# Performance work log

Hardware: AMD Instinct MI355X
Metric: run time of the kernel (lower is better)

The kernel has to match this reference:

```python
import jax, jax.numpy as jnp
import numpy as np

W, H = 512, 512
SHIFT_NORM = 100.0
P = 1
WEIGHT = 10.0
EPS = 1e-16


def _cv_matrix(angle, scale, shift, cx, cy):
    # cv2.getRotationMatrix2D-style matrix (pixel coords) with extra x-shift.
    alpha = scale * jnp.cos(angle)
    beta = scale * jnp.sin(angle)
    row0 = jnp.stack([alpha, beta, (1.0 - alpha) * cx - beta * cy + shift], axis=-1)
    row1 = jnp.stack([-beta, alpha, beta * cx + (1.0 - alpha) * cy], axis=-1)
    return jnp.stack([row0, row1], axis=-2)  # [B,2,3]


def _normalize_transform(M, width, height):
    # Convert pixel-space affine to normalized [-1,1] coords (align_corners=True).
    a, b, tx = M[:, 0, 0], M[:, 0, 1], M[:, 0, 2]
    c, d, ty = M[:, 1, 0], M[:, 1, 1], M[:, 1, 2]
    sw = float(width - 1)
    sh = float(height - 1)
    A = a
    Bc = b * sh / sw
    Cc = a + b * sh / sw + 2.0 * tx / sw - 1.0
    D = c * sw / sh
    E = d
    Fc = c * sw / sh + d + 2.0 * ty / sh - 1.0
    row0 = jnp.stack([A, Bc, Cc], axis=-1)
    row1 = jnp.stack([D, E, Fc], axis=-1)
    return jnp.stack([row0, row1], axis=-2)  # [B,2,3]


def _affine_grid(T, height, width):
    # torch affine_grid, align_corners=True
    u = jnp.linspace(-1.0, 1.0, width, dtype=T.dtype)
    v = jnp.linspace(-1.0, 1.0, height, dtype=T.dtype)
    vv, uu = jnp.meshgrid(v, u, indexing='ij')
    base = jnp.stack([uu, vv, jnp.ones_like(uu)], axis=-1)  # [H,W,3]
    return jnp.einsum('bij,hwj->bhwi', T, base)  # [B,H,W,2] (x,y)


def _grid_sample(img, grid):
    # bilinear, zeros padding, align_corners=True. img [B,C,H,W], grid [B,Ho,Wo,2]
    B, C, Hi, Wi = img.shape
    x = (grid[..., 0] + 1.0) * (Wi - 1) / 2.0
    y = (grid[..., 1] + 1.0) * (Hi - 1) / 2.0
    x0 = jnp.floor(x)
    y0 = jnp.floor(y)
    wx1 = x - x0
    wy1 = y - y0
    wx0 = 1.0 - wx1
    wy0 = 1.0 - wy1

    def gather(xi, yi):
        valid = ((xi >= 0) & (xi < Wi) & (yi >= 0) & (yi < Hi)).astype(img.dtype)
        xc = jnp.clip(xi, 0, Wi - 1).astype(jnp.int32)
        yc = jnp.clip(yi, 0, Hi - 1).astype(jnp.int32)
        g = jax.vmap(lambda im, xb, yb, vb: im[:, yb, xb] * vb[None])
        return g(img, xc, yc, valid)  # [B,C,Ho,Wo]

    out = (gather(x0, y0) * (wx0 * wy0)[:, None]
           + gather(x0 + 1, y0) * (wx1 * wy0)[:, None]
           + gather(x0, y0 + 1) * (wx0 * wy1)[:, None]
           + gather(x0 + 1, y0 + 1) * (wx1 * wy1)[:, None])
    return out


def setup_inputs() -> dict:
    key = jax.random.key(0)
    k1, k2, k3 = jax.random.split(key, 3)
    theta = jax.random.normal(k1, (32, 3), dtype=jnp.float32)
    img_R = jax.random.normal(k2, (32, 3, H, W), dtype=jnp.float32)
    img_R_orig = jax.random.normal(k3, (32, 3, H, W), dtype=jnp.float32)
    return {"theta": theta, "img_R": img_R, "img_R_orig": img_R_orig}


def reference(theta, img_R, img_R_orig):
    cx, cy = W // 2, H // 2
    M = _cv_matrix(theta[:, 0], theta[:, 1], SHIFT_NORM * theta[:, 2], cx, cy)
    T = _normalize_transform(M, W, H)
    grid = _affine_grid(T, H, W)
    warped = _grid_sample(img_R_orig, grid)
    mask = jnp.ones((img_R.shape[0], 1, H, W), dtype=img_R.dtype)
    warped_mask = _grid_sample(mask, grid)[:, 0]  # [B,H,W]
    # p=1 norm over channel dim
    nrm = jnp.sum(jnp.abs(img_R - warped), axis=1)  # [B,H,W]
    num = jnp.sum(warped_mask * nrm, axis=(1, 2)) + EPS
    den = jnp.sum(warped_mask, axis=(1, 2)) + EPS
    losses = WEIGHT * num / den
    return jnp.mean(losses)
```

## Files before the change

### kernel.cpp

```cpp
#include <hip/hip_runtime.h>
#include <math.h>

#define IMG_W 512
#define IMG_H 512
#define NB 32
#define NC 3
#define PLANE (IMG_H * IMG_W)

#define TILE_W 32
#define TILE_H 32
#define TILES_X (IMG_W / TILE_W)
#define TILES_Y (IMG_H / TILE_H)
#define TILES_PER_B (TILES_X * TILES_Y)
#define NBLOCKS (NB * TILES_PER_B)

#define LDSF 6144

typedef float vfloat4 __attribute__((ext_vector_type(4)));


__global__ __launch_bounds__(256) void recon_main(
    const float* __restrict__ theta,
    const float* __restrict__ img_R,
    const float* __restrict__ img_orig,
    float* __restrict__ ws)
{
    __shared__ __align__(16) float tileLds[LDSF];
    __shared__ float snum[4];
    __shared__ float sden[4];

    const int lin = blockIdx.x;
    const int xcd = lin & 7;
    const int loc = lin >> 3;
    const int b   = xcd * 4 + (loc >> 8);
    const int tile = loc & 255;
    const int tx = (tile & (TILES_X - 1)) * TILE_W;
    const int ty = (tile >> 4) * TILE_H;

    const int tid  = threadIdx.x;
    const int trow = tid >> 3;
    const int tcol = (tid & 7) * 4;

    const float ang   = theta[b * 3 + 0];
    const float s     = theta[b * 3 + 1];
    const float shift = 100.0f * theta[b * 3 + 2];
    float sn, cs;
    sincosf(ang, &sn, &cs);
    const float alpha = s * cs;
    const float beta  = s * sn;
    const float tx_a = (1.0f - alpha) * 256.0f - beta * 256.0f + shift;
    const float ty_a = beta * 256.0f + (1.0f - alpha) * 256.0f;
    const float Cc = alpha + beta + 2.0f * tx_a / 511.0f - 1.0f;
    const float Fc = -beta + alpha + 2.0f * ty_a / 511.0f - 1.0f;
    const float X0 = 255.5f * (Cc + 1.0f - alpha - beta);
    const float Y0 = 255.5f * (Fc + 1.0f + beta - alpha);

    const float* orig_b = img_orig + (size_t)b * NC * PLANE;
    const float* R_b    = img_R    + (size_t)b * NC * PLANE;

    const int h  = ty + trow;
    const int w0 = tx + tcol;
    const int p0 = h * IMG_W + w0;

    const float xb = X0 + alpha * (float)w0 + beta * (float)h;
    const float yb = Y0 - beta * (float)w0 + alpha * (float)h;

    int   xi0a[4], xi1a[4], yi0a[4], yi1a[4];
    float w00[4], w10[4], w01[4], w11[4], mk[4];
    float den_acc = 0.0f;

#pragma unroll
    for (int j = 0; j < 4; ++j) {
        const float x = xb + alpha * (float)j;
        const float y = yb - beta  * (float)j;
        const float x0f = floorf(x), y0f = floorf(y);
        const float fx1 = x - x0f,  fy1 = y - y0f;
        const float fx0 = 1.0f - fx1, fy0 = 1.0f - fy1;
        const float vx0 = (x0f >=  0.0f && x0f <= 511.0f) ? 1.0f : 0.0f;
        const float vx1 = (x0f >= -1.0f && x0f <= 510.0f) ? 1.0f : 0.0f;
        const float vy0 = (y0f >=  0.0f && y0f <= 511.0f) ? 1.0f : 0.0f;
        const float vy1 = (y0f >= -1.0f && y0f <= 510.0f) ? 1.0f : 0.0f;
        xi0a[j] = (int)fminf(fmaxf(x0f,        0.0f), 511.0f);
        xi1a[j] = (int)fminf(fmaxf(x0f + 1.0f, 0.0f), 511.0f);
        yi0a[j] = (int)fminf(fmaxf(y0f,        0.0f), 511.0f);
        yi1a[j] = (int)fminf(fmaxf(y0f + 1.0f, 0.0f), 511.0f);
        w00[j] = fx0 * fy0 * vx0 * vy0;
        w10[j] = fx1 * fy0 * vx1 * vy0;
        w01[j] = fx0 * fy1 * vx0 * vy1;
        w11[j] = fx1 * fy1 * vx1 * vy1;
        mk[j]  = w00[j] + w10[j] + w01[j] + w11[j];
        den_acc += mk[j];
    }

    const float fx_lo = (float)tx, fx_hi = (float)(tx + TILE_W - 1);
    const float fy_lo = (float)ty, fy_hi = (float)(ty + TILE_H - 1);
    const float cxA = X0 + alpha * fx_lo + beta * fy_lo;
    const float cxB = X0 + alpha * fx_hi + beta * fy_lo;
    const float cxC = X0 + alpha * fx_lo + beta * fy_hi;
    const float cxD = X0 + alpha * fx_hi + beta * fy_hi;
    const float cyA = Y0 - beta * fx_lo + alpha * fy_lo;
    const float cyB = Y0 - beta * fx_hi + alpha * fy_lo;
    const float cyC = Y0 - beta * fx_lo + alpha * fy_hi;
    const float cyD = Y0 - beta * fx_hi + alpha * fy_hi;
    const float min_x = fminf(fminf(cxA, cxB), fminf(cxC, cxD));
    const float max_x = fmaxf(fmaxf(cxA, cxB), fmaxf(cxC, cxD));
    const float min_y = fminf(fminf(cyA, cyB), fminf(cyC, cyD));
    const float max_y = fmaxf(fmaxf(cyA, cyB), fmaxf(cyC, cyD));

    int xlo = (int)floorf(min_x);
    int xhi = (int)floorf(max_x) + 1;
    xlo = min(max(xlo, 0), 511);
    xhi = min(max(xhi, 0), 511);
    xlo &= ~3;
    int ylo = (int)floorf(min_y);
    int yhi = (int)floorf(max_y) + 1;
    ylo = min(max(ylo, 0), 511);
    yhi = min(max(yhi, 0), 511);

    const int bw = xhi - xlo + 1;
    const int bh = yhi - ylo + 1;
    int stride = (bw + 3) & ~3;
    if (((stride >> 2) & 1) == 0) stride += 4;
    const int nq4 = stride >> 2;
    const bool staged = (stride * bh <= LDSF) && (nq4 <= 32);

    float nrm[4] = {0.0f, 0.0f, 0.0f, 0.0f};

    if (staged) {
        int l00[4], l10[4], l01[4], l11[4];
#pragma unroll
        for (int j = 0; j < 4; ++j) {
            const int r0 = (yi0a[j] - ylo) * stride - xlo;
            const int r1 = (yi1a[j] - ylo) * stride - xlo;
            l00[j] = r0 + xi0a[j];
            l10[j] = r0 + xi1a[j];
            l01[j] = r1 + xi0a[j];
            l11[j] = r1 + xi1a[j];
        }
        const int qq  = tid & 31;
        const int r00 = tid >> 5;
        const int col = xlo + (qq << 2);
        const bool doload = (col <= xhi);

        for (int c = 0; c < NC; ++c) {
            if (c) __syncthreads();
            const float* plane = orig_b + c * PLANE;
            if (doload) {
                for (int r = r00; r < bh; r += 8) {
                    const vfloat4 v = *(const vfloat4*)(plane + (ylo + r) * IMG_W + col);
                    *(vfloat4*)(&tileLds[r * stride + (qq << 2)]) = v;
                }
            }
            __syncthreads();
            const vfloat4 rv = __builtin_nontemporal_load(
                                 (const vfloat4*)(R_b + c * PLANE + p0));
            const float rj[4] = {rv.x, rv.y, rv.z, rv.w};
#pragma unroll
            for (int j = 0; j < 4; ++j) {
                const float s00 = tileLds[l00[j]];
                const float s10 = tileLds[l10[j]];
                const float s01 = tileLds[l01[j]];
                const float s11 = tileLds[l11[j]];
                const float warped = s00 * w00[j] + s10 * w10[j]
                                   + s01 * w01[j] + s11 * w11[j];
                nrm[j] += fabsf(rj[j] - warped);
            }
        }
    } else {
        int a0[4], a1[4], sl0[4], sl1[4];
#pragma unroll
        for (int j = 0; j < 4; ++j) {
            const int xc = min(xi0a[j], 510);
            a0[j]  = yi0a[j] * IMG_W + xc;
            a1[j]  = yi1a[j] * IMG_W + xc;
            sl0[j] = xi0a[j] - xc;
            sl1[j] = xi1a[j] - xc;
        }
#pragma unroll
        for (int c = 0; c < NC; ++c) {
            const float* plane = orig_b + c * PLANE;
            const vfloat4 rv = __builtin_nontemporal_load(
                                 (const vfloat4*)(R_b + c * PLANE + p0));
            const float rj[4] = {rv.x, rv.y, rv.z, rv.w};
#pragma unroll
            for (int j = 0; j < 4; ++j) {
                const float2 t0 = *(const float2*)(plane + a0[j]);
                const float2 t1 = *(const float2*)(plane + a1[j]);
                const float s00 = sl0[j] ? t0.y : t0.x;
                const float s10 = sl1[j] ? t0.y : t0.x;
                const float s01 = sl0[j] ? t1.y : t1.x;
                const float s11 = sl1[j] ? t1.y : t1.x;
                const float warped = s00 * w00[j] + s10 * w10[j]
                                   + s01 * w01[j] + s11 * w11[j];
                nrm[j] += fabsf(rj[j] - warped);
            }
        }
    }

    float num_acc = 0.0f;
#pragma unroll
    for (int j = 0; j < 4; ++j) num_acc += mk[j] * nrm[j];

#pragma unroll
    for (int off = 32; off > 0; off >>= 1) {
        num_acc += __shfl_down(num_acc, off);
        den_acc += __shfl_down(den_acc, off);
    }

    const int wave = threadIdx.x >> 6;
    const int lane = threadIdx.x & 63;
    if (lane == 0) { snum[wave] = num_acc; sden[wave] = den_acc; }
    __syncthreads();
    if (threadIdx.x == 0) {
        ws[lin]           = snum[0] + snum[1] + snum[2] + snum[3];
        ws[NBLOCKS + lin] = sden[0] + sden[1] + sden[2] + sden[3];
    }
}

__global__ __launch_bounds__(256) void recon_final(
    const float* __restrict__ ws,
    float* __restrict__ out)
{
    __shared__ float sloss[NB];
    const int t = threadIdx.x;
    const int b = t >> 3;
    const int j = t & 7;

    float n = 0.0f, d = 0.0f;
    for (int k = 0; k < 32; ++k) {
        const int tile = j * 32 + k;
        const int lin  = ((b & 3) * 256 + tile) * 8 + (b >> 2);
        n += ws[lin];
        d += ws[NBLOCKS + lin];
    }
#pragma unroll
    for (int off = 4; off > 0; off >>= 1) {
        n += __shfl_down(n, off);
        d += __shfl_down(d, off);
    }
    if (j == 0) sloss[b] = 10.0f * (n + 1e-16f) / (d + 1e-16f);
    __syncthreads();
    if (t == 0) {
        float L = 0.0f;
#pragma unroll
        for (int i = 0; i < NB; ++i) L += sloss[i];
        out[0] = L * (1.0f / (float)NB);
    }
}

extern "C" void kernel_launch(void* const* d_in, const int* in_sizes, int n_in,
                              void* d_out, int out_size, void* d_ws, size_t ws_size,
                              hipStream_t stream) {
    const float* theta    = (const float*)d_in[0];
    const float* img_R    = (const float*)d_in[1];
    const float* img_orig = (const float*)d_in[2];
    float* out = (float*)d_out;
    float* ws  = (float*)d_ws;

    recon_main<<<NBLOCKS, 256, 0, stream>>>(theta, img_R, img_orig, ws);
    recon_final<<<1, 256, 0, stream>>>(ws, out);
}
```

Measured before the change: 253.0 us.

## Skip out-of-image tiles, add interior fast path and all-channel LDS staging

Whole-tile early exit is added when the tile's source footprint falls completely outside the image, writing zero partials. Tiles whose footprint is fully interior get a fast path with no validity masks or clamping. A new tier stages all three channels into LDS with a single barrier when they fit, and the old per-channel staging remains as a second tier. Block-to-(batch,tile) mapping is changed to batch-fastest interleaving instead of the XCD-aware mapping, which may affect L2 locality.

```diff
diff --git a/kernel.cpp b/kernel.cpp
--- a/kernel.cpp
+++ b/kernel.cpp
@@ -10,8 +10,7 @@
 #define TILE_W 32
 #define TILE_H 32
 #define TILES_X (IMG_W / TILE_W)
-#define TILES_Y (IMG_H / TILE_H)
-#define TILES_PER_B (TILES_X * TILES_Y)
+#define TILES_PER_B 256
 #define NBLOCKS (NB * TILES_PER_B)
 
 #define LDSF 6144
@@ -29,11 +28,9 @@
     __shared__ float snum[4];
     __shared__ float sden[4];
 
-    const int lin = blockIdx.x;
-    const int xcd = lin & 7;
-    const int loc = lin >> 3;
-    const int b   = xcd * 4 + (loc >> 8);
-    const int tile = loc & 255;
+    const int lin  = blockIdx.x;
+    const int b    = lin & (NB - 1);
+    const int tile = lin >> 5;
     const int tx = (tile & (TILES_X - 1)) * TILE_W;
     const int ty = (tile >> 4) * TILE_H;
 
@@ -54,43 +51,6 @@
     const float Fc = -beta + alpha + 2.0f * ty_a / 511.0f - 1.0f;
     const float X0 = 255.5f * (Cc + 1.0f - alpha - beta);
     const float Y0 = 255.5f * (Fc + 1.0f + beta - alpha);
-
-    const float* orig_b = img_orig + (size_t)b * NC * PLANE;
-    const float* R_b    = img_R    + (size_t)b * NC * PLANE;
-
-    const int h  = ty + trow;
-    const int w0 = tx + tcol;
-    const int p0 = h * IMG_W + w0;
-
-    const float xb = X0 + alpha * (float)w0 + beta * (float)h;
-    const float yb = Y0 - beta * (float)w0 + alpha * (float)h;
-
-    int   xi0a[4], xi1a[4], yi0a[4], yi1a[4];
-    float w00[4], w10[4], w01[4], w11[4], mk[4];
-    float den_acc = 0.0f;
-
-#pragma unroll
-    for (int j = 0; j < 4; ++j) {
-        const float x = xb + alpha * (float)j;
-        const float y = yb - beta  * (float)j;
-        const float x0f = floorf(x), y0f = floorf(y);
-        const float fx1 = x - x0f,  fy1 = y - y0f;
-        const float fx0 = 1.0f - fx1, fy0 = 1.0f - fy1;
-        const float vx0 = (x0f >=  0.0f && x0f <= 511.0f) ? 1.0f : 0.0f;
-        const float vx1 = (x0f >= -1.0f && x0f <= 510.0f) ? 1.0f : 0.0f;
-        const float vy0 = (y0f >=  0.0f && y0f <= 511.0f) ? 1.0f : 0.0f;
-        const float vy1 = (y0f >= -1.0f && y0f <= 510.0f) ? 1.0f : 0.0f;
-        xi0a[j] = (int)fminf(fmaxf(x0f,        0.0f), 511.0f);
-        xi1a[j] = (int)fminf(fmaxf(x0f + 1.0f, 0.0f), 511.0f);
-        yi0a[j] = (int)fminf(fmaxf(y0f,        0.0f), 511.0f);
-        yi1a[j] = (int)fminf(fmaxf(y0f + 1.0f, 0.0f), 511.0f);
-        w00[j] = fx0 * fy0 * vx0 * vy0;
-        w10[j] = fx1 * fy0 * vx1 * vy0;
-        w01[j] = fx0 * fy1 * vx0 * vy1;
-        w11[j] = fx1 * fy1 * vx1 * vy1;
-        mk[j]  = w00[j] + w10[j] + w01[j] + w11[j];
-        den_acc += mk[j];
-    }
 
     const float fx_lo = (float)tx, fx_hi = (float)(tx + TILE_W - 1);
     const float fy_lo = (float)ty, fy_hi = (float)(ty + TILE_H - 1);
@@ -107,13 +67,21 @@
     const float min_y = fminf(fminf(cyA, cyB), fminf(cyC, cyD));
     const float max_y = fmaxf(fmaxf(cyA, cyB), fmaxf(cyC, cyD));
 
-    int xlo = (int)floorf(min_x);
-    int xhi = (int)floorf(max_x) + 1;
+    if (max_x < -1.01f || min_x > 512.01f || max_y < -1.01f || min_y > 512.01f) {
+        if (tid == 0) { ws[lin] = 0.0f; ws[NBLOCKS + lin] = 0.0f; }
+        return;
+    }
+
+    const bool interior = (min_x > 0.5f) && (max_x < 510.0f) &&
+                          (min_y > 0.5f) && (max_y < 510.0f);
+
+    int xlo = (int)floorf(min_x) - 1;
+    int xhi = (int)floorf(max_x) + 2;
     xlo = min(max(xlo, 0), 511);
     xhi = min(max(xhi, 0), 511);
     xlo &= ~3;
-    int ylo = (int)floorf(min_y);
-    int yhi = (int)floorf(max_y) + 1;
+    int ylo = (int)floorf(min_y) - 1;
+    int yhi = (int)floorf(max_y) + 2;
     ylo = min(max(ylo, 0), 511);
     yhi = min(max(yhi, 0), 511);
 
@@ -122,34 +90,127 @@
     int stride = (bw + 3) & ~3;
     if (((stride >> 2) & 1) == 0) stride += 4;
     const int nq4 = stride >> 2;
-    const bool staged = (stride * bh <= LDSF) && (nq4 <= 32);
+    const int sb = stride * bh;
+    const bool okw   = (nq4 <= 32);
+    const bool tier1 = okw && (3 * sb <= LDSF);
+    const bool tier2 = okw && !tier1 && (sb <= LDSF);
+
+    const float* orig_b = img_orig + (size_t)b * NC * PLANE;
+    const float* R_b    = img_R    + (size_t)b * NC * PLANE;
+
+    const int h  = ty + trow;
+    const int w0 = tx + tcol;
+    const int p0 = h * IMG_W + w0;
+
+    const float xb = X0 + alpha * (float)w0 + beta * (float)h;
+    const float yb = Y0 - beta * (float)w0 + alpha * (float)h;
+
+    int   xcA[4], yi0a[4], yi1a[4], sl0[4], sl1[4];
+    float w00[4], w10[4], w01[4], w11[4], mk[4];
+    float den_acc = 0.0f;
+
+    if (interior) {
+#pragma unroll
+        for (int j = 0; j < 4; ++j) {
+            const float x = xb + alpha * (float)j;
+            const float y = yb - beta  * (float)j;
+            const float x0f = floorf(x), y0f = floorf(y);
+            const float fx1 = x - x0f,  fy1 = y - y0f;
+            const float fx0 = 1.0f - fx1, fy0 = 1.0f - fy1;
+            const int xi0 = (int)x0f, yi0 = (int)y0f;
+            xcA[j] = xi0; yi0a[j] = yi0; yi1a[j] = yi0 + 1;
+            sl0[j] = 0;   sl1[j] = 1;
+            w00[j] = fx0 * fy0; w10[j] = fx1 * fy0;
+            w01[j] = fx0 * fy1; w11[j] = fx1 * fy1;
+            mk[j]  = 1.0f;
+            den_acc += 1.0f;
+        }
+    } else {
+#pragma unroll
+        for (int j = 0; j < 4; ++j) {
+            const float x = xb + alpha * (float)j;
+            const float y = yb - beta  * (float)j;
+            const float x0f = floorf(x), y0f = floorf(y);
+            const float fx1 = x - x0f,  fy1 = y - y0f;
+            const float fx0 = 1.0f - fx1, fy0 = 1.0f - fy1;
+            const float vx0 = (x0f >=  0.0f && x0f <= 511.0f) ? 1.0f : 0.0f;
+            const float vx1 = (x0f >= -1.0f && x0f <= 510.0f) ? 1.0f : 0.0f;
+            const float vy0 = (y0f >=  0.0f && y0f <= 511.0f) ? 1.0f : 0.0f;
+            const float vy1 = (y0f >= -1.0f && y0f <= 510.0f) ? 1.0f : 0.0f;
+            const int xi0 = (int)fminf(fmaxf(x0f,        0.0f), 511.0f);
+            const int xi1 = (int)fminf(fmaxf(x0f + 1.0f, 0.0f), 511.0f);
+            yi0a[j] = (int)fminf(fmaxf(y0f,        0.0f), 511.0f);
+            yi1a[j] = (int)fminf(fmaxf(y0f + 1.0f, 0.0f), 511.0f);
+            const int xc = min(xi0, 510);
+            xcA[j] = xc; sl0[j] = xi0 - xc; sl1[j] = xi1 - xc;
+            w00[j] = fx0 * fy0 * vx0 * vy0;
+            w10[j] = fx1 * fy0 * vx1 * vy0;
+            w01[j] = fx0 * fy1 * vx0 * vy1;
+            w11[j] = fx1 * fy1 * vx1 * vy1;
+            mk[j]  = w00[j] + w10[j] + w01[j] + w11[j];
+            den_acc += mk[j];
+        }
+    }
 
     float nrm[4] = {0.0f, 0.0f, 0.0f, 0.0f};
 
-    if (staged) {
-        int l00[4], l10[4], l01[4], l11[4];
-#pragma unroll
-        for (int j = 0; j < 4; ++j) {
-            const int r0 = (yi0a[j] - ylo) * stride - xlo;
-            const int r1 = (yi1a[j] - ylo) * stride - xlo;
-            l00[j] = r0 + xi0a[j];
-            l10[j] = r0 + xi1a[j];
-            l01[j] = r1 + xi0a[j];
-            l11[j] = r1 + xi1a[j];
+    if (tier1) {
+        int l0[4], l1[4];
+#pragma unroll
+        for (int j = 0; j < 4; ++j) {
+            l0[j] = (yi0a[j] - ylo) * stride + (xcA[j] - xlo);
+            l1[j] = (yi1a[j] - ylo) * stride + (xcA[j] - xlo);
+        }
+        const int qq  = tid & 31;
+        const int r00 = tid >> 5;
+        const int col = xlo + (qq << 2);
+        if (col <= xhi) {
+            for (int c = 0; c < NC; ++c) {
+                const float* plane = orig_b + c * PLANE;
+                float* dst = tileLds + c * sb;
+                for (int r = r00; r < bh; r += 8)
+                    *(vfloat4*)(dst + r * stride + (qq << 2)) =
+                        *(const vfloat4*)(plane + (ylo + r) * IMG_W + col);
+            }
+        }
+        __syncthreads();
+#pragma unroll
+        for (int c = 0; c < NC; ++c) {
+            const float* lsrc = tileLds + c * sb;
+            const vfloat4 rv = __builtin_nontemporal_load(
+                                 (const vfloat4*)(R_b + c * PLANE + p0));
+            const float rj[4] = {rv.x, rv.y, rv.z, rv.w};
+#pragma unroll
+            for (int j = 0; j < 4; ++j) {
+                const float u0 = lsrc[l0[j]], u1 = lsrc[l0[j] + 1];
+                const float v0 = lsrc[l1[j]], v1 = lsrc[l1[j] + 1];
+                const float s00 = sl0[j] ? u1 : u0;
+                const float s10 = sl1[j] ? u1 : u0;
+                const float s01 = sl0[j] ? v1 : v0;
+                const float s11 = sl1[j] ? v1 : v0;
+                const float warped = s00 * w00[j] + s10 * w10[j]
+                                   + s01 * w01[j] + s11 * w11[j];
+                nrm[j] += fabsf(rj[j] - warped);
+            }
+        }
+    } else if (tier2) {
+        int l0[4], l1[4];
+#pragma unroll
+        for (int j = 0; j < 4; ++j) {
+            l0[j] = (yi0a[j] - ylo) * stride + (xcA[j] - xlo);
+            l1[j] = (yi1a[j] - ylo) * stride + (xcA[j] - xlo);
         }
         const int qq  = tid & 31;
         const int r00 = tid >> 5;
         const int col = xlo + (qq << 2);
         const bool doload = (col <= xhi);
-
         for (int c = 0; c < NC; ++c) {
             if (c) __syncthreads();
             const float* plane = orig_b + c * PLANE;
             if (doload) {
-                for (int r = r00; r < bh; r += 8) {
-                    const vfloat4 v = *(const vfloat4*)(plane + (ylo + r) * IMG_W + col);
-                    *(vfloat4*)(&tileLds[r * stride + (qq << 2)]) = v;
-                }
+                for (int r = r00; r < bh; r += 8)
+                    *(vfloat4*)(&tileLds[r * stride + (qq << 2)]) =
+                        *(const vfloat4*)(plane + (ylo + r) * IMG_W + col);
             }
             __syncthreads();
             const vfloat4 rv = __builtin_nontemporal_load(
@@ -157,24 +218,23 @@
             const float rj[4] = {rv.x, rv.y, rv.z, rv.w};
 #pragma unroll
             for (int j = 0; j < 4; ++j) {
-                const float s00 = tileLds[l00[j]];
-                const float s10 = tileLds[l10[j]];
-                const float s01 = tileLds[l01[j]];
-                const float s11 = tileLds[l11[j]];
+                const float u0 = tileLds[l0[j]], u1 = tileLds[l0[j] + 1];
+                const float v0 = tileLds[l1[j]], v1 = tileLds[l1[j] + 1];
+                const float s00 = sl0[j] ? u1 : u0;
+                const float s10 = sl1[j] ? u1 : u0;
+                const float s01 = sl0[j] ? v1 : v0;
+                const float s11 = sl1[j] ? v1 : v0;
                 const float warped = s00 * w00[j] + s10 * w10[j]
                                    + s01 * w01[j] + s11 * w11[j];
                 nrm[j] += fabsf(rj[j] - warped);
             }
         }
     } else {
-        int a0[4], a1[4], sl0[4], sl1[4];
-#pragma unroll
-        for (int j = 0; j < 4; ++j) {
-            const int xc = min(xi0a[j], 510);
-            a0[j]  = yi0a[j] * IMG_W + xc;
-            a1[j]  = yi1a[j] * IMG_W + xc;
-            sl0[j] = xi0a[j] - xc;
-            sl1[j] = xi1a[j] - xc;
+        int a0[4], a1[4];
+#pragma unroll
+        for (int j = 0; j < 4; ++j) {
+            a0[j] = yi0a[j] * IMG_W + xcA[j];
+            a1[j] = yi1a[j] * IMG_W + xcA[j];
         }
 #pragma unroll
         for (int c = 0; c < NC; ++c) {
@@ -207,11 +267,11 @@
         den_acc += __shfl_down(den_acc, off);
     }
 
-    const int wave = threadIdx.x >> 6;
-    const int lane = threadIdx.x & 63;
+    const int wave = tid >> 6;
+    const int lane = tid & 63;
     if (lane == 0) { snum[wave] = num_acc; sden[wave] = den_acc; }
     __syncthreads();
-    if (threadIdx.x == 0) {
+    if (tid == 0) {
         ws[lin]           = snum[0] + snum[1] + snum[2] + snum[3];
         ws[NBLOCKS + lin] = sden[0] + sden[1] + sden[2] + sden[3];
     }
@@ -229,7 +289,7 @@
     float n = 0.0f, d = 0.0f;
     for (int k = 0; k < 32; ++k) {
         const int tile = j * 32 + k;
-        const int lin  = ((b & 3) * 256 + tile) * 8 + (b >> 2);
+        const int lin  = tile * NB + b;
         n += ws[lin];
         d += ws[NBLOCKS + lin];
     }
```

Result: slower. 268.6 us (+6.2%).
